# Optimization experiments

Hardware: AMD Instinct MI355X
Metric: run time of the kernel (lower is better)

The kernel has to match this reference:

```python
import jax, jax.numpy as jnp
import numpy as np
import math

B, P, PIX, D, C = 128, 256, 256, 512, 10
MAX_STEPS, TOL, EPS = 4, 1e-3, 1e-5


def setup_inputs() -> dict:
    key = jax.random.key(0)
    ks = jax.random.split(key, 12)
    pi = math.pi
    return {
        "x": jax.random.normal(ks[0], (B, P, PIX), jnp.float32),
        "Wp": jax.random.normal(ks[1], (D, PIX), jnp.float32) * (1.0 / math.sqrt(PIX)),
        "bp": jnp.zeros((D,), jnp.float32),
        "q_rot": jax.random.uniform(ks[2], (D,), jnp.float32, -pi, pi),
        "k_rot": jax.random.uniform(ks[3], (D,), jnp.float32, -pi, pi),
        "v_rot": jax.random.uniform(ks[4], (D,), jnp.float32, -pi, pi),
        "ff_real": jax.random.normal(ks[5], (D, D), jnp.float32) * (1.0 / math.sqrt(D)),
        "ff_imag": jax.random.uniform(ks[6], (D, D), jnp.float32, -0.01, 0.01),
        "Wr": jax.random.normal(ks[7], (C, D), jnp.float32) * 0.05,
        "br": jnp.zeros((C,), jnp.float32),
        "Wi": jax.random.normal(ks[8], (C, D), jnp.float32) * 0.05,
        "bi": jnp.zeros((C,), jnp.float32),
    }


def _complex_norm(x):
    # normalize magnitude stats over last dim, preserve phase (torch.std uses ddof=1)
    mag = jnp.abs(x)
    mean_mag = jnp.mean(mag, axis=-1, keepdims=True)
    std_mag = jnp.std(mag, axis=-1, keepdims=True, ddof=1)
    norm_mag = (mag - mean_mag) / (std_mag + EPS)
    scale = jnp.tanh(norm_mag) / (mag + EPS)
    return x * scale


def _fro(z):
    return jnp.sqrt(jnp.sum(jnp.abs(z) ** 2))


def _pos_phase():
    pos = jnp.arange(P, dtype=jnp.float32)[:, None]
    dim = jnp.arange(D, dtype=jnp.float32)[None, :]
    freq = 1.0 / (10000.0 ** (dim / D))
    return pos * freq * math.pi  # (P, D)


def reference(x, Wp, bp, q_rot, k_rot, v_rot, ff_real, ff_imag, Wr, br, Wi, bi):
    mag = jnp.tanh(jnp.einsum('bpi,di->bpd', x, Wp) + bp)
    state = mag.astype(jnp.complex64) * jnp.exp(1j * _pos_phase())[None]  # (B,P,D)
    ff = (ff_real + 1j * ff_imag).astype(jnp.complex64)
    eq, ek, ev = jnp.exp(1j * q_rot), jnp.exp(1j * k_rot), jnp.exp(1j * v_rot)
    scale = 8.0 / math.sqrt(D)
    active = jnp.array(True)
    for _ in range(MAX_STEPS):  # fixed small iteration count; updates frozen after convergence
        prev = state
        q, k, v = state * eq, state * ek, state * ev
        interference = jnp.einsum('bpd,bqd->bpq', q, jnp.conj(k))
        attn = jax.nn.softmax(interference.real * scale, axis=-1)
        attn_out = jnp.einsum('bpq,bqd->bpd', attn.astype(jnp.complex64), v)
        new_state = _complex_norm((prev + attn_out) @ ff)
        diff = _fro(new_state - prev) / (_fro(new_state) + 1e-8)
        state = jnp.where(active, new_state, prev)
        active = jnp.logical_and(active, diff >= TOL)
    pooled = jnp.mean(state, axis=1)  # (B,D) complex
    logits = pooled.real @ Wr.T + br + pooled.imag @ Wi.T + bi
    return logits
```

## Files before the change

kernel.cpp:

```cpp
#include <hip/hip_runtime.h>
#include <math.h>

#define BB   128
#define PP   256
#define PIX_ 256
#define DD   512
#define CC   10
#define MTOT (BB*PP)
#define NK   1024
#define KA   2048
#define KB2  2048
#define NSLOT (MTOT/4)

static constexpr float SCALE_F = 0.35355339059327373f;
static constexpr float PI_F    = 3.14159265358979323846f;

typedef short bf16x8 __attribute__((ext_vector_type(8)));
typedef float f32x4  __attribute__((ext_vector_type(4)));
typedef unsigned short ushort8 __attribute__((ext_vector_type(8)));

__device__ __forceinline__ unsigned short f2bf(float f) {
    union { float f; unsigned u; } v; v.f = f;
    unsigned r = v.u + 0x7FFF + ((v.u >> 16) & 1);
    return (unsigned short)(r >> 16);
}
__device__ __forceinline__ float bf2f(unsigned short h) {
    union { unsigned u; float f; } v; v.u = ((unsigned)h) << 16;
    return v.f;
}

typedef __attribute__((address_space(3))) unsigned lds_u32;
typedef __attribute__((address_space(1))) const unsigned glb_u32;
__device__ __forceinline__ void gl2lds16(const unsigned short* g, short* l) {
    __builtin_amdgcn_global_load_lds((glb_u32*)g, (lds_u32*)l, 16, 0, 0);
}

__global__ void k_setup(const float* __restrict__ q_rot, const float* __restrict__ k_rot,
                        const float* __restrict__ v_rot,
                        float* __restrict__ freq, float* __restrict__ cd, float* __restrict__ sd,
                        float* __restrict__ cv, float* __restrict__ sv,
                        int* __restrict__ active) {
    int t = threadIdx.x;
    if (t < DD) {
        freq[t] = expf(-(float)t * (9.210340371976184f / 512.0f));
        float dl = q_rot[t] - k_rot[t];
        cd[t] = cosf(dl);       sd[t] = sinf(dl);
        cv[t] = cosf(v_rot[t]); sv[t] = sinf(v_rot[t]);
    }
    if (t == 0) *active = 1;
}

__global__ __launch_bounds__(256) void k_tab(const float* __restrict__ freq,
                                             float* __restrict__ Tc, float* __restrict__ Ts) {
    const int p = blockIdx.x, t = threadIdx.x;
#pragma unroll
    for (int j = 0; j < 2; j++) {
        const int d = t * 2 + j;
        float s, c; sincosf((float)p * freq[d] * PI_F, &s, &c);
        Tc[(size_t)p * DD + d] = c;
        Ts[(size_t)p * DD + d] = s;
    }
}

__global__ __launch_bounds__(256) void k_prep2(const float* __restrict__ Fr, const float* __restrict__ Fi,
                                               unsigned short* __restrict__ Bt2) {
    const int n = blockIdx.x;
    const int t = threadIdx.x;
    unsigned short* row = Bt2 + (size_t)n * KB2;
#pragma unroll
    for (int j4 = 0; j4 < 4; j4++) {
        const int j = j4 * 256 + t;
        float v;
        if (n < 512) v = (j < 512) ? Fr[(size_t)j * DD + n] : -Fi[(size_t)(j - 512) * DD + n];
        else         v = (j < 512) ? Fi[(size_t)j * DD + (n - 512)] : Fr[(size_t)(j - 512) * DD + (n - 512)];
        const unsigned short hi = f2bf(v);
        row[j] = hi;
        row[NK + j] = f2bf(v - bf2f(hi));
    }
}

#define SCAT4(TILE, V4) do { TILE[lk+0][lrow]=(V4).x; TILE[lk+1][lrow]=(V4).y; \
                             TILE[lk+2][lrow]=(V4).z; TILE[lk+3][lrow]=(V4).w; } while(0)

__global__ __launch_bounds__(256) void k_init(const float* __restrict__ x,
        const float* __restrict__ Wp, const float* __restrict__ bp,
        const float* __restrict__ Tc, const float* __restrict__ Ts,
        float* Sr, float* Si,
        unsigned short* X, unsigned short* Y,
        const float* __restrict__ cd, const float* __restrict__ sd,
        const int packed) {
    __shared__ float As[16][68];
    __shared__ float Bs[16][68];
    const int bm = blockIdx.y * 64, bn = blockIdx.x * 64;
    const int t = threadIdx.x, tx = t & 15, ty = t >> 4;
    const int lrow = t >> 2, lk = (t & 3) * 4;
    float acc[4][4] = {};
    for (int k0 = 0; k0 < PIX_; k0 += 16) {
        const float4 a4 = *(const float4*)(x  + (size_t)(bm + lrow) * PIX_ + k0 + lk);
        const float4 b4 = *(const float4*)(Wp + (size_t)(bn + lrow) * PIX_ + k0 + lk);
        __syncthreads();
        SCAT4(As, a4);
        SCAT4(Bs, b4);
        __syncthreads();
#pragma unroll
        for (int kk = 0; kk < 16; ++kk) {
            const float4 av = *(const float4*)&As[kk][ty * 4];
            const float4 bv = *(const float4*)&Bs[kk][tx * 4];
            const float a[4] = {av.x, av.y, av.z, av.w};
            const float b[4] = {bv.x, bv.y, bv.z, bv.w};
#pragma unroll
            for (int i = 0; i < 4; i++)
#pragma unroll
                for (int j = 0; j < 4; j++) acc[i][j] = fmaf(a[i], b[j], acc[i][j]);
        }
    }
    const float4 cd4 = *(const float4*)(cd + bn + tx * 4);
    const float4 sd4 = *(const float4*)(sd + bn + tx * 4);
    const float cdv[4] = {cd4.x, cd4.y, cd4.z, cd4.w};
    const float sdv[4] = {sd4.x, sd4.y, sd4.z, sd4.w};
#pragma unroll
    for (int i = 0; i < 4; i++) {
        const int m = bm + ty * 4 + i;
        const int p = m & 255;
        const float4 c4 = *(const float4*)(Tc + (size_t)p * DD + bn + tx * 4);
        const float4 s4 = *(const float4*)(Ts + (size_t)p * DD + bn + tx * 4);
        const float cphv[4] = {c4.x, c4.y, c4.z, c4.w};
        const float sphv[4] = {s4.x, s4.y, s4.z, s4.w};
        float srv[4], siv[4];
#pragma unroll
        for (int j = 0; j < 4; j++) {
            const int d = bn + tx * 4 + j;
            const float mg = tanhf(acc[i][j] + bp[d]);
            srv[j] = mg * cphv[j]; siv[j] = mg * sphv[j];
        }
        if (packed) {
            ushort4 xhr, xhi, xlr, xli, yhr, yhi, ylr, yli;
            unsigned short* po[8] = {(unsigned short*)&xhr, (unsigned short*)&xhi,
                                     (unsigned short*)&xlr, (unsigned short*)&xli,
                                     (unsigned short*)&yhr, (unsigned short*)&yhi,
                                     (unsigned short*)&ylr, (unsigned short*)&yli};
#pragma unroll
            for (int j = 0; j < 4; j++) {
                const unsigned short hr = f2bf(srv[j]);
                const unsigned short hi_ = f2bf(siv[j]);
                po[0][j] = hr;  po[2][j] = f2bf(srv[j] - bf2f(hr));
                po[1][j] = hi_; po[3][j] = f2bf(siv[j] - bf2f(hi_));
                const float krr = srv[j] * cdv[j] + siv[j] * sdv[j];
                const float kri = siv[j] * cdv[j] - srv[j] * sdv[j];
                const unsigned short y1 = f2bf(krr);
                const unsigned short y2 = f2bf(kri);
                po[4][j] = y1; po[6][j] = f2bf(krr - bf2f(y1));
                po[5][j] = y2; po[7][j] = f2bf(kri - bf2f(y2));
            }
            unsigned short* xr = X + (size_t)m * KA + bn + tx * 4;
            unsigned short* yr = Y + (size_t)m * KA + bn + tx * 4;
            *(ushort4*)(xr)        = xhr; *(ushort4*)(xr + 512)  = xhi;
            *(ushort4*)(xr + 1024) = xlr; *(ushort4*)(xr + 1536) = xli;
            *(ushort4*)(yr)        = yhr; *(ushort4*)(yr + 512)  = yhi;
            *(ushort4*)(yr + 1024) = ylr; *(ushort4*)(yr + 1536) = yli;
        } else {
            float4 vr, vi;
            float* pvr = (float*)&vr; float* pvi = (float*)&vi;
#pragma unroll
            for (int j = 0; j < 4; j++) { pvr[j] = srv[j]; pvi[j] = siv[j]; }
            *(float4*)(Sr + (size_t)m * DD + bn + tx * 4) = vr;
            *(float4*)(Si + (size_t)m * DD + bn + tx * 4) = vi;
        }
    }
}

__global__ __launch_bounds__(256) void k_xy(const float* __restrict__ Sr, const float* __restrict__ Si,
        const float* __restrict__ cd, const float* __restrict__ sd,
        unsigned short* X, unsigned short* Y,
        const int* __restrict__ active) {
    if (*active == 0) return;
    const int r = blockIdx.x, t = threadIdx.x;
    const size_t base = (size_t)r * DD + 2 * t;
    const float2 s_r = *(const float2*)(Sr + base);
    const float2 s_i = *(const float2*)(Si + base);
    const float2 c2  = *(const float2*)(cd + 2 * t);
    const float2 s2  = *(const float2*)(sd + 2 * t);
    unsigned short* xr = X + (size_t)r * KA;
    unsigned short* yr = Y + (size_t)r * KA;
    const float srv[2] = {s_r.x, s_r.y}, siv[2] = {s_i.x, s_i.y};
    const float cv_[2] = {c2.x, c2.y},  sv_[2] = {s2.x, s2.y};
    ushort2 xh_r, xh_i, xl_r, xl_i, yh_r, yh_i, yl_r, yl_i;
    unsigned short* o[8] = {(unsigned short*)&xh_r, (unsigned short*)&xh_i,
                            (unsigned short*)&xl_r, (unsigned short*)&xl_i,
                            (unsigned short*)&yh_r, (unsigned short*)&yh_i,
                            (unsigned short*)&yl_r, (unsigned short*)&yl_i};
#pragma unroll
    for (int e = 0; e < 2; e++) {
        const unsigned short hr = f2bf(srv[e]);
        const unsigned short hi_ = f2bf(siv[e]);
        o[0][e] = hr;  o[2][e] = f2bf(srv[e] - bf2f(hr));
        o[1][e] = hi_; o[3][e] = f2bf(siv[e] - bf2f(hi_));
        const float krr = srv[e] * cv_[e] + siv[e] * sv_[e];
        const float kri = siv[e] * cv_[e] - srv[e] * sv_[e];
        const unsigned short yh1 = f2bf(krr);
        const unsigned short yh2 = f2bf(kri);
        o[4][e] = yh1; o[6][e] = f2bf(krr - bf2f(yh1));
        o[5][e] = yh2; o[7][e] = f2bf(kri - bf2f(yh2));
    }
    *(ushort2*)(xr + 2 * t)        = xh_r;
    *(ushort2*)(xr + 512 + 2 * t)  = xh_i;
    *(ushort2*)(xr + 1024 + 2 * t) = xl_r;
    *(ushort2*)(xr + 1536 + 2 * t) = xl_i;
    *(ushort2*)(yr + 2 * t)        = yh_r;
    *(ushort2*)(yr + 512 + 2 * t)  = yh_i;
    *(ushort2*)(yr + 1024 + 2 * t) = yl_r;
    *(ushort2*)(yr + 1536 + 2 * t) = yl_i;
}

__global__ __launch_bounds__(256) void k_score_sm(const unsigned short* __restrict__ X,
        const unsigned short* __restrict__ Y,
        unsigned short* __restrict__ Asp, const int* __restrict__ active) {
    if (*active == 0) return;
    __shared__ short SM[20480];
    short* XH = SM;
    short* XL = SM + 2048;
    short* YH = SM + 4096;
    short* YL = SM + 12288;
    const int t = threadIdx.x;
    const int w = t >> 6, L = t & 63;
    const int lane15 = L & 15, quad = L >> 4;
    const int nsm = (int)gridDim.x >> 2;
    const int s   = (int)blockIdx.x & (nsm - 1);
    const int rt  = (int)blockIdx.x / nsm;
    const int bm = s * 256 + rt * 64;
    const int yb = s * 256;
    const int gr = t >> 2, ch = (t & 3) * 8;
    short* XHw = XH + w * 512;
    short* XLw = XL + w * 512;
    short* YHw = YH + w * 512;
    short* YLw = YL + w * 512;
    f32x4 acc[16] = {};
    for (int k0 = 0; k0 < 1024; k0 += 32) {
        __syncthreads();
        gl2lds16(X + (size_t)(bm + gr) * KA + k0 + ch,        XHw);
        gl2lds16(X + (size_t)(bm + gr) * KA + 1024 + k0 + ch, XLw);
#pragma unroll
        for (int ss = 0; ss < 4; ss++) {
            gl2lds16(Y + (size_t)(yb + ss * 64 + gr) * KA + k0 + ch,        YHw + ss * 2048);
            gl2lds16(Y + (size_t)(yb + ss * 64 + gr) * KA + 1024 + k0 + ch, YLw + ss * 2048);
        }
        __syncthreads();
        const bf16x8 xh = *(const bf16x8*)(XH + (w * 16 + lane15) * 32 + quad * 8);
        const bf16x8 xl = *(const bf16x8*)(XL + (w * 16 + lane15) * 32 + quad * 8);
#pragma unroll
        for (int tc = 0; tc < 16; tc++) {
            const bf16x8 yh = *(const bf16x8*)(YH + (tc * 16 + lane15) * 32 + quad * 8);
            acc[tc] = __builtin_amdgcn_mfma_f32_16x16x32_bf16(xh, yh, acc[tc], 0, 0, 0);
            acc[tc] = __builtin_amdgcn_mfma_f32_16x16x32_bf16(xl, yh, acc[tc], 0, 0, 0);
            const bf16x8 yl = *(const bf16x8*)(YL + (tc * 16 + lane15) * 32 + quad * 8);
            acc[tc] = __builtin_amdgcn_mfma_f32_16x16x32_bf16(xh, yl, acc[tc], 0, 0, 0);
        }
    }
#pragma unroll
    for (int tc = 0; tc < 16; tc++) acc[tc] *= SCALE_F;
#pragma unroll
    for (int r = 0; r < 4; r++) {
        float mx = acc[0][r];
#pragma unroll
        for (int tc = 1; tc < 16; tc++) mx = fmaxf(mx, acc[tc][r]);
#pragma unroll
        for (int off = 8; off; off >>= 1) mx = fmaxf(mx, __shfl_xor(mx, off, 64));
        float sum = 0.f;
#pragma unroll
        for (int tc = 0; tc < 16; tc++) { acc[tc][r] = __expf(acc[tc][r] - mx); sum += acc[tc][r]; }
#pragma unroll
        for (int off = 8; off; off >>= 1) sum += __shfl_xor(sum, off, 64);
        const float inv = 1.0f / sum;
#pragma unroll
        for (int tc = 0; tc < 16; tc++) acc[tc][r] *= inv;
    }
    __syncthreads();
#pragma unroll
    for (int h = 0; h < 2; h++) {
        if ((w >> 1) == h) {
#pragma unroll
            for (int r = 0; r < 4; r++) {
                const int lr = (w & 1) * 16 + quad * 4 + r;
#pragma unroll
                for (int tc = 0; tc < 16; tc++) {
                    const float p = acc[tc][r];
                    const unsigned short hi = f2bf(p);
                    SM[lr * 520 + tc * 16 + lane15] = (short)hi;
                    SM[lr * 520 + 256 + tc * 16 + lane15] = (short)f2bf(p - bf2f(hi));
                }
            }
        }
        __syncthreads();
        unsigned short* dst = Asp + (size_t)(bm + h * 32) * 512;
#pragma unroll
        for (int k = 0; k < 8; k++) {
            const int c = t + 256 * k;
            const int row = c >> 6, off = (c & 63) * 8;
            *(ushort8*)(dst + (size_t)c * 8) = *(const ushort8*)&SM[row * 520 + off];
        }
        __syncthreads();
    }
}

__global__ __launch_bounds__(256) void k_attnout_mfma(const unsigned short* __restrict__ Asp,
        const unsigned short* __restrict__ X,
        const float* __restrict__ cv, const float* __restrict__ sv,
        unsigned short* __restrict__ A2, const int* __restrict__ active) {
    if (*active == 0) return;
    __shared__ short AhT[128][32];
    __shared__ short AlT[128][32];
    __shared__ short BH[128][40];
    __shared__ short BL[128][40];
    const int t = threadIdx.x;
    const int w = t >> 6, L = t & 63;
    const int lane15 = L & 15, quad = L >> 4;
    const int bm = blockIdx.x * 128;
    const int bn = blockIdx.y * 64;
    const int sample = blockIdx.x >> 1;
    const int gr = t >> 2, ch = (t & 3) * 8;
    short* AhW0 = &AhT[0][0] + w * 512;
    short* AhW1 = AhW0 + 64 * 32;
    short* AlW0 = &AlT[0][0] + w * 512;
    short* AlW1 = AlW0 + 64 * 32;
    const int nn = t & 127, kh = t >> 7;
    const unsigned short* Bsrc = X + (size_t)sample * PP * KA
                               + ((nn < 64) ? (bn + nn) : (512 + bn + nn - 64));
    f32x4 acc[2][8] = {};
    for (int q0 = 0; q0 < PP; q0 += 32) {
        __syncthreads();
        gl2lds16(Asp + (size_t)(bm + gr) * 512      + q0 + ch,       AhW0);
        gl2lds16(Asp + (size_t)(bm + 64 + gr) * 512 + q0 + ch,       AhW1);
        gl2lds16(Asp + (size_t)(bm + gr) * 512      + 256 + q0 + ch, AlW0);
        gl2lds16(Asp + (size_t)(bm + 64 + gr) * 512 + 256 + q0 + ch, AlW1);
#pragma unroll
        for (int kg = 0; kg < 2; kg++) {
            const int qb = kh * 16 + kg * 8;
            bf16x8 hh, ll;
#pragma unroll
            for (int j = 0; j < 8; j++) {
                const size_t o = (size_t)(q0 + qb + j) * KA;
                hh[j] = (short)Bsrc[o];
                ll[j] = (short)Bsrc[o + 1024];
            }
            *(bf16x8*)&BH[nn][qb] = hh;
            *(bf16x8*)&BL[nn][qb] = ll;
        }
        __syncthreads();
        bf16x8 bh[8];
#pragma unroll
        for (int tc = 0; tc < 8; tc++)
            bh[tc] = *(const bf16x8*)&BH[tc * 16 + lane15][quad * 8];
        bf16x8 afh[2];
#pragma unroll
        for (int tr = 0; tr < 2; tr++) {
            afh[tr] = *(const bf16x8*)&AhT[w * 32 + tr * 16 + lane15][quad * 8];
            const bf16x8 afl = *(const bf16x8*)&AlT[w * 32 + tr * 16 + lane15][quad * 8];
#pragma unroll
            for (int tc = 0; tc < 8; tc++)
                acc[tr][tc] = __builtin_amdgcn_mfma_f32_16x16x32_bf16(afh[tr], bh[tc], acc[tr][tc], 0, 0, 0);
#pragma unroll
            for (int tc = 0; tc < 8; tc++)
                acc[tr][tc] = __builtin_amdgcn_mfma_f32_16x16x32_bf16(afl, bh[tc], acc[tr][tc], 0, 0, 0);
        }
#pragma unroll
        for (int tc = 0; tc < 8; tc++) {
            const bf16x8 bl = *(const bf16x8*)&BL[tc * 16 + lane15][quad * 8];
            acc[0][tc] = __builtin_amdgcn_mfma_f32_16x16x32_bf16(afh[0], bl, acc[0][tc], 0, 0, 0);
            acc[1][tc] = __builtin_amdgcn_mfma_f32_16x16x32_bf16(afh[1], bl, acc[1][tc], 0, 0, 0);
        }
    }
#pragma unroll
    for (int tr = 0; tr < 2; tr++) {
#pragma unroll
        for (int tc = 0; tc < 4; tc++) {
            const int d = bn + tc * 16 + lane15;
            const float cvd = cv[d], svd = sv[d];
#pragma unroll
            for (int r = 0; r < 4; r++) {
                const int m = bm + w * 32 + tr * 16 + quad * 4 + r;
                const unsigned short* xrow = X + (size_t)m * KA + d;
                const float pvr = bf2f(xrow[0])   + bf2f(xrow[1024]);
                const float pvi = bf2f(xrow[512]) + bf2f(xrow[1536]);
                const float wr = acc[tr][tc][r];
                const float wi = acc[tr][tc + 4][r];
                const float tr_ = pvr + (wr * cvd - wi * svd);
                const float ti_ = pvi + (wr * svd + wi * cvd);
                const unsigned short rh = f2bf(tr_);
                const unsigned short ih = f2bf(ti_);
                unsigned short* arow = A2 + (size_t)m * KA;
                arow[d]        = rh;
                arow[512 + d]  = ih;
                arow[1024 + d] = f2bf(tr_ - bf2f(rh));
                arow[1536 + d] = f2bf(ti_ - bf2f(ih));
            }
        }
    }
}

__global__ __launch_bounds__(256) void k_ff_mfma2(const unsigned short* __restrict__ A2,
        const unsigned short* __restrict__ Bt2,
        float* __restrict__ U, const int* __restrict__ active) {
    if (*active == 0) return;
    __shared__ short AH[128][32], AL[128][32];
    __shared__ short BH[128][32], BL[128][32];
    const int t = threadIdx.x;
    const int w = t >> 6, L = t & 63;
    const int lane15 = L & 15, quad = L >> 4;
    const int bm = blockIdx.x * 128, bn = blockIdx.y * 128;
    const int gr = t >> 2, ch = (t & 3) * 8;
    short* AHw = &AH[0][0] + w * 512;
    short* ALw = &AL[0][0] + w * 512;
    short* BHw = &BH[0][0] + w * 512;
    short* BLw = &BL[0][0] + w * 512;
    f32x4 acc[2][8] = {};
    for (int k0 = 0; k0 < 1024; k0 += 32) {
        __syncthreads();
        gl2lds16(A2  + (size_t)(bm + gr) * KA       + k0 + ch,        AHw);
        gl2lds16(A2  + (size_t)(bm + 64 + gr) * KA  + k0 + ch,        AHw + 64 * 32);
        gl2lds16(A2  + (size_t)(bm + gr) * KA       + 1024 + k0 + ch, ALw);
        gl2lds16(A2  + (size_t)(bm + 64 + gr) * KA  + 1024 + k0 + ch, ALw + 64 * 32);
        gl2lds16(Bt2 + (size_t)(bn + gr) * KB2      + k0 + ch,        BHw);
        gl2lds16(Bt2 + (size_t)(bn + 64 + gr) * KB2 + k0 + ch,        BHw + 64 * 32);
        gl2lds16(Bt2 + (size_t)(bn + gr) * KB2      + 1024 + k0 + ch, BLw);
        gl2lds16(Bt2 + (size_t)(bn + 64 + gr) * KB2 + 1024 + k0 + ch, BLw + 64 * 32);
        __syncthreads();
        bf16x8 ah[2], al[2];
#pragma unroll
        for (int tr = 0; tr < 2; tr++) {
            ah[tr] = *(const bf16x8*)&AH[w * 32 + tr * 16 + lane15][quad * 8];
            al[tr] = *(const bf16x8*)&AL[w * 32 + tr * 16 + lane15][quad * 8];
        }
#pragma unroll
        for (int tc = 0; tc < 8; tc++) {
            const bf16x8 bh = *(const bf16x8*)&BH[tc * 16 + lane15][quad * 8];
            acc[0][tc] = __builtin_amdgcn_mfma_f32_16x16x32_bf16(ah[0], bh, acc[0][tc], 0, 0, 0);
            acc[1][tc] = __builtin_amdgcn_mfma_f32_16x16x32_bf16(ah[1], bh, acc[1][tc], 0, 0, 0);
            acc[0][tc] = __builtin_amdgcn_mfma_f32_16x16x32_bf16(al[0], bh, acc[0][tc], 0, 0, 0);
            acc[1][tc] = __builtin_amdgcn_mfma_f32_16x16x32_bf16(al[1], bh, acc[1][tc], 0, 0, 0);
            const bf16x8 bl = *(const bf16x8*)&BL[tc * 16 + lane15][quad * 8];
            acc[0][tc] = __builtin_amdgcn_mfma_f32_16x16x32_bf16(ah[0], bl, acc[0][tc], 0, 0, 0);
            acc[1][tc] = __builtin_amdgcn_mfma_f32_16x16x32_bf16(ah[1], bl, acc[1][tc], 0, 0, 0);
        }
    }
#pragma unroll
    for (int tr = 0; tr < 2; tr++)
#pragma unroll
        for (int tc = 0; tc < 8; tc++) {
            const int n = bn + tc * 16 + lane15;
            const int mbase = bm + w * 32 + tr * 16 + quad * 4;
#pragma unroll
            for (int r = 0; r < 4; r++)
                U[(size_t)(mbase + r) * NK + n] = acc[tr][tc][r];
        }
}

__global__ __launch_bounds__(256) void k_norm(const float* U,
        float* Sr, float* Si,
        float* __restrict__ part,
        unsigned short* X, unsigned short* Y,
        const float* __restrict__ cd, const float* __restrict__ sd,
        const int mode, const int* __restrict__ active) {
    if (*active == 0) return;
    __shared__ float red[8];
    const int t = threadIdx.x, rt = t >> 6, L = t & 63;
    const int row = blockIdx.x * 4 + rt;
    const size_t ub = (size_t)row * NK;
    const size_t base = (size_t)row * DD;
    const float4 ur0 = *(const float4*)(U + ub + 4 * L);
    const float4 ur1 = *(const float4*)(U + ub + 256 + 4 * L);
    const float4 ui0 = *(const float4*)(U + ub + 512 + 4 * L);
    const float4 ui1 = *(const float4*)(U + ub + 768 + 4 * L);
    float prr[8], pii[8];
    unsigned short* xr = X + (size_t)row * KA;
    if (mode == 2) {
        const ushort4 hr0 = *(const ushort4*)(xr + 4 * L);
        const ushort4 hr1 = *(const ushort4*)(xr + 256 + 4 * L);
        const ushort4 hi0 = *(const ushort4*)(xr + 512 + 4 * L);
        const ushort4 hi1 = *(const ushort4*)(xr + 768 + 4 * L);
        const ushort4 lr0 = *(const ushort4*)(xr + 1024 + 4 * L);
        const ushort4 lr1 = *(const ushort4*)(xr + 1280 + 4 * L);
        const ushort4 li0 = *(const ushort4*)(xr + 1536 + 4 * L);
        const ushort4 li1 = *(const ushort4*)(xr + 1792 + 4 * L);
        const unsigned short* hr[2] = {(const unsigned short*)&hr0, (const unsigned short*)&hr1};
        const unsigned short* hi[2] = {(const unsigned short*)&hi0, (const unsigned short*)&hi1};
        const unsigned short* lr[2] = {(const unsigned short*)&lr0, (const unsigned short*)&lr1};
        const unsigned short* li[2] = {(const unsigned short*)&li0, (const unsigned short*)&li1};
#pragma unroll
        for (int e = 0; e < 8; e++) {
            const int g = e >> 2, j = e & 3;
            prr[e] = bf2f(hr[g][j]) + bf2f(lr[g][j]);
            pii[e] = bf2f(hi[g][j]) + bf2f(li[g][j]);
        }
    } else {
        const float4 pr0 = *(const float4*)(Sr + base + 4 * L);
        const float4 pr1 = *(const float4*)(Sr + base + 256 + 4 * L);
        const float4 pi0 = *(const float4*)(Si + base + 4 * L);
        const float4 pi1 = *(const float4*)(Si + base + 256 + 4 * L);
        prr[0] = pr0.x; prr[1] = pr0.y; prr[2] = pr0.z; prr[3] = pr0.w;
        prr[4] = pr1.x; prr[5] = pr1.y; prr[6] = pr1.z; prr[7] = pr1.w;
        pii[0] = pi0.x; pii[1] = pi0.y; pii[2] = pi0.z; pii[3] = pi0.w;
        pii[4] = pi1.x; pii[5] = pi1.y; pii[6] = pi1.z; pii[7] = pi1.w;
    }
    const float urr[8] = {ur0.x, ur0.y, ur0.z, ur0.w, ur1.x, ur1.y, ur1.z, ur1.w};
    const float uii[8] = {ui0.x, ui0.y, ui0.z, ui0.w, ui1.x, ui1.y, ui1.z, ui1.w};
    float mg[8], msum = 0.f;
#pragma unroll
    for (int e = 0; e < 8; e++) {
        mg[e] = sqrtf(urr[e] * urr[e] + uii[e] * uii[e]);
        msum += mg[e];
    }
#pragma unroll
    for (int off = 32; off; off >>= 1) msum += __shfl_xor(msum, off, 64);
    const float mean = msum * (1.0f / 512.0f);
    float vs = 0.f;
#pragma unroll
    for (int e = 0; e < 8; e++) { const float d = mg[e] - mean; vs += d * d; }
#pragma unroll
    for (int off = 32; off; off >>= 1) vs += __shfl_xor(vs, off, 64);
    const float istd = 1.0f / (sqrtf(vs * (1.0f / 511.0f)) + 1e-5f);
    float nr[8], ni[8];
#pragma unroll
    for (int e = 0; e < 8; e++) {
        const float sc = tanhf((mg[e] - mean) * istd) / (mg[e] + 1e-5f);
        nr[e] = urr[e] * sc; ni[e] = uii[e] * sc;
    }
    float dd = 0.f, nn = 0.f;
#pragma unroll
    for (int e = 0; e < 8; e++) {
        const float dr = nr[e] - prr[e], di = ni[e] - pii[e];
        dd += dr * dr + di * di;
        nn += nr[e] * nr[e] + ni[e] * ni[e];
    }
    if (mode != 2) {
        *(float4*)(Sr + base + 4 * L)       = make_float4(nr[0], nr[1], nr[2], nr[3]);
        *(float4*)(Sr + base + 256 + 4 * L) = make_float4(nr[4], nr[5], nr[6], nr[7]);
        *(float4*)(Si + base + 4 * L)       = make_float4(ni[0], ni[1], ni[2], ni[3]);
        *(float4*)(Si + base + 256 + 4 * L) = make_float4(ni[4], ni[5], ni[6], ni[7]);
    }
    if (mode >= 1) {
        unsigned short* yr = Y + (size_t)row * KA;
        const float4 c0 = *(const float4*)(cd + 4 * L);
        const float4 c1 = *(const float4*)(cd + 256 + 4 * L);
        const float4 s0 = *(const float4*)(sd + 4 * L);
        const float4 s1 = *(const float4*)(sd + 256 + 4 * L);
        const float cdv[8] = {c0.x, c0.y, c0.z, c0.w, c1.x, c1.y, c1.z, c1.w};
        const float sdv[8] = {s0.x, s0.y, s0.z, s0.w, s1.x, s1.y, s1.z, s1.w};
        ushort4 xhr[2], xhi[2], xlr[2], xli[2], yhr[2], yhi[2], ylr[2], yli[2];
#pragma unroll
        for (int e = 0; e < 8; e++) {
            const int g = e >> 2, j = e & 3;
            const unsigned short hr_ = f2bf(nr[e]);
            const unsigned short hi_ = f2bf(ni[e]);
            ((unsigned short*)&xhr[g])[j] = hr_;
            ((unsigned short*)&xlr[g])[j] = f2bf(nr[e] - bf2f(hr_));
            ((unsigned short*)&xhi[g])[j] = hi_;
            ((unsigned short*)&xli[g])[j] = f2bf(ni[e] - bf2f(hi_));
            const float krr = nr[e] * cdv[e] + ni[e] * sdv[e];
            const float kri = ni[e] * cdv[e] - nr[e] * sdv[e];
            const unsigned short k1 = f2bf(krr);
            const unsigned short k2 = f2bf(kri);
            ((unsigned short*)&yhr[g])[j] = k1;
            ((unsigned short*)&ylr[g])[j] = f2bf(krr - bf2f(k1));
            ((unsigned short*)&yhi[g])[j] = k2;
            ((unsigned short*)&yli[g])[j] = f2bf(kri - bf2f(k2));
        }
        *(ushort4*)(xr + 4 * L)        = xhr[0]; *(ushort4*)(xr + 256 + 4 * L)  = xhr[1];
        *(ushort4*)(xr + 512 + 4 * L)  = xhi[0]; *(ushort4*)(xr + 768 + 4 * L)  = xhi[1];
        *(ushort4*)(xr + 1024 + 4 * L) = xlr[0]; *(ushort4*)(xr + 1280 + 4 * L) = xlr[1];
        *(ushort4*)(xr + 1536 + 4 * L) = xli[0]; *(ushort4*)(xr + 1792 + 4 * L) = xli[1];
        *(ushort4*)(yr + 4 * L)        = yhr[0]; *(ushort4*)(yr + 256 + 4 * L)  = yhr[1];
        *(ushort4*)(yr + 512 + 4 * L)  = yhi[0]; *(ushort4*)(yr + 768 + 4 * L)  = yhi[1];
        *(ushort4*)(yr + 1024 + 4 * L) = ylr[0]; *(ushort4*)(yr + 1280 + 4 * L) = ylr[1];
        *(ushort4*)(yr + 1536 + 4 * L) = yli[0]; *(ushort4*)(yr + 1792 + 4 * L) = yli[1];
    }
#pragma unroll
    for (int off = 32; off; off >>= 1) {
        dd += __shfl_xor(dd, off, 64);
        nn += __shfl_xor(nn, off, 64);
    }
    if (L == 0) { red[rt] = dd; red[4 + rt] = nn; }
    __syncthreads();
    if (t == 0)
        *(float2*)(part + 2 * blockIdx.x) =
            make_float2(red[0] + red[1] + red[2] + red[3],
                        red[4] + red[5] + red[6] + red[7]);
}

__global__ __launch_bounds__(256) void k_flag(const float* __restrict__ part, int* __restrict__ active) {
    __shared__ float red[8];
    const int t = threadIdx.x, rt = t >> 6, L = t & 63;
    float dd = 0.f, nn = 0.f;
    for (int i = t; i < NSLOT; i += 256) {
        const float2 p = *(const float2*)(part + 2 * i);
        dd += p.x; nn += p.y;
    }
#pragma unroll
    for (int off = 32; off; off >>= 1) {
        dd += __shfl_xor(dd, off, 64);
        nn += __shfl_xor(nn, off, 64);
    }
    if (L == 0) { red[rt] = dd; red[4 + rt] = nn; }
    __syncthreads();
    if (t == 0) {
        const float d = red[0] + red[1] + red[2] + red[3];
        const float n = red[4] + red[5] + red[6] + red[7];
        const float diff = sqrtf(d) / (sqrtf(n) + 1e-8f);
        const int a = *active;
        *active = (a && (diff >= 1e-3f)) ? 1 : 0;
    }
}

__global__ __launch_bounds__(256) void k_pool(const float* __restrict__ Sr, const float* __restrict__ Si,
        const unsigned short* __restrict__ X,
        float* __restrict__ Pr, float* __restrict__ Pi, const int packed) {
    const int gid = blockIdx.x * 256 + threadIdx.x;
    const int b = gid >> 9, d = gid & 511;
    float sr = 0.f, si = 0.f;
    if (packed) {
        const unsigned short* xb = X + ((size_t)b * PP) * KA + d;
        for (int p = 0; p < PP; p++) {
            const unsigned short* xr = xb + (size_t)p * KA;
            sr += bf2f(xr[0])   + bf2f(xr[1024]);
            si += bf2f(xr[512]) + bf2f(xr[1536]);
        }
    } else {
        const size_t base = (size_t)b * PP * DD + d;
        for (int p = 0; p < PP; p++) {
            sr += Sr[base + (size_t)p * DD];
            si += Si[base + (size_t)p * DD];
        }
    }
    Pr[gid] = sr * (1.0f / 256.0f);
    Pi[gid] = si * (1.0f / 256.0f);
}

__global__ __launch_bounds__(64) void k_logits(const float* __restrict__ Pr, const float* __restrict__ Pi,
        const float* __restrict__ Wr, const float* __restrict__ br,
        const float* __restrict__ Wi, const float* __restrict__ bi,
        float* __restrict__ out) {
    const int b = blockIdx.x;
    const int lane = threadIdx.x;
    for (int c = 0; c < CC; c++) {
        float acc = 0.f;
#pragma unroll
        for (int k = 0; k < 8; k++) {
            const int d = lane + 64 * k;
            acc += Pr[b * DD + d] * Wr[c * DD + d] + Pi[b * DD + d] * Wi[c * DD + d];
        }
#pragma unroll
        for (int off = 32; off; off >>= 1) acc += __shfl_xor(acc, off, 64);
        if (lane == 0) out[b * CC + c] = acc + br[c] + bi[c];
    }
}

extern "C" void kernel_launch(void* const* d_in, const int* in_sizes, int n_in,
                              void* d_out, int out_size, void* d_ws, size_t ws_size,
                              hipStream_t stream) {
    const float* x     = (const float*)d_in[0];
    const float* Wp    = (const float*)d_in[1];
    const float* bp    = (const float*)d_in[2];
    const float* q_rot = (const float*)d_in[3];
    const float* k_rot = (const float*)d_in[4];
    const float* v_rot = (const float*)d_in[5];
    const float* ffr   = (const float*)d_in[6];
    const float* ffi   = (const float*)d_in[7];
    const float* Wr    = (const float*)d_in[8];
    const float* br    = (const float*)d_in[9];
    const float* Wi    = (const float*)d_in[10];
    const float* bi    = (const float*)d_in[11];
    float* out = (float*)d_out;

    float* ws = (float*)d_ws;
    const size_t plane = (size_t)MTOT * DD;
    const size_t sline = (size_t)PP * DD;

    float* freq = ws;
    float* cd   = freq + DD;
    float* sd   = cd + DD;
    float* cv   = sd + DD;
    float* sv   = cv + DD;
    int*   active = (int*)(sv + DD);
    float* Pr = ws + 4096;
    float* Pi = Pr + (size_t)BB * DD;
    float* part = Pi + (size_t)BB * DD;

    const size_t headf = 151552;
    const size_t btf   = (size_t)NK * KB2 / 2;
    const size_t tabf  = 2 * (size_t)PP * DD;
    const size_t xf    = (size_t)MTOT * KA / 2;
    const size_t packed_f = headf + btf + tabf + 3 * xf;
    const int packed = ((packed_f * 4ull) <= ws_size);

    k_setup<<<1, 512, 0, stream>>>(q_rot, k_rot, v_rot, freq, cd, sd, cv, sv, active);

    if (packed) {
        unsigned short* Bt2 = (unsigned short*)(ws + headf);
        float* Tc = (float*)(Bt2 + (size_t)NK * KB2);
        float* Ts = Tc + (size_t)PP * DD;
        unsigned short* X = (unsigned short*)(Ts + (size_t)PP * DD);
        unsigned short* Y = X + (size_t)MTOT * KA;
        unsigned short* Asp = Y + (size_t)MTOT * KA;
        unsigned short* A2 = Y;
        float* U = (float*)Asp;

        k_tab<<<PP, 256, 0, stream>>>(freq, Tc, Ts);
        k_prep2<<<NK, 256, 0, stream>>>(ffr, ffi, Bt2);
        k_init<<<dim3(DD / 64, MTOT / 64), 256, 0, stream>>>(x, Wp, bp, Tc, Ts,
                nullptr, nullptr, X, Y, cd, sd, 1);

        for (int it = 0; it < 4; ++it) {
            k_score_sm<<<BB * 4, 256, 0, stream>>>(X, Y, Asp, active);
            k_attnout_mfma<<<dim3(BB * 2, 8), 256, 0, stream>>>(Asp, X, cv, sv, A2, active);
            k_ff_mfma2<<<dim3(BB * 2, NK / 128), 256, 0, stream>>>(A2, Bt2, U, active);
            k_norm<<<BB * (PP / 4), 256, 0, stream>>>(U, nullptr, nullptr, part, X, Y, cd, sd, 2, active);
            k_flag<<<1, 256, 0, stream>>>(part, active);
        }
        k_pool<<<BB * DD / 256, 256, 0, stream>>>(nullptr, nullptr, X, Pr, Pi, 1);
    } else {
        float* Sr = part + 2 * NSLOT;
        float* Si = Sr + plane;
        unsigned short* Bt2 = (unsigned short*)(Si + plane);
        float* Tc = (float*)(Bt2 + (size_t)NK * KB2);
        float* Ts = Tc + (size_t)PP * DD;
        float* chunkbase = Si + plane + (size_t)NK * 3072 / 2;

        const size_t fixed_f = (4096 + 2 * (size_t)BB * DD + 2 * NSLOT) + 2 * plane + (size_t)NK * 3072 / 2;
        const size_t perC_f = (size_t)PP * NK * 2 + (size_t)PP * 256;

        int C = BB;
        while (C > 1 && (fixed_f + (size_t)C * perC_f) * 4ull > ws_size) C >>= 1;
        const int fullXY = (C == BB);

        float* U = chunkbase;
        unsigned short* X  = (unsigned short*)chunkbase;
        float* Yf = chunkbase + (size_t)C * PP * NK;
        unsigned short* Y  = (unsigned short*)Yf;
        unsigned short* A2 = Y;
        unsigned short* Asp = (unsigned short*)(Yf + (size_t)C * PP * NK);

        k_tab<<<PP, 256, 0, stream>>>(freq, Tc, Ts);
        k_prep2<<<NK, 256, 0, stream>>>(ffr, ffi, Bt2);
        k_init<<<dim3(DD / 64, MTOT / 64), 256, 0, stream>>>(x, Wp, bp, Tc, Ts,
                Sr, Si, nullptr, nullptr, cd, sd, 0);

        for (int it = 0; it < 4; ++it) {
            for (int c0 = 0; c0 < BB; c0 += C) {
                float* Sr_c = Sr + (size_t)c0 * sline;
                float* Si_c = Si + (size_t)c0 * sline;
                float* part_c = part + (size_t)c0 * (PP / 4) * 2;
                if (!fullXY || it == 0)
                    k_xy<<<C * PP, 256, 0, stream>>>(Sr_c, Si_c, cd, sd, X, Y, active);
                k_score_sm<<<C * 4, 256, 0, stream>>>(X, Y, Asp, active);
                k_attnout_mfma<<<dim3(C * 2, 8), 256, 0, stream>>>(Asp, X, cv, sv, A2, active);
                k_ff_mfma2<<<dim3(C * 2, NK / 128), 256, 0, stream>>>(A2, Bt2, U, active);
                k_norm<<<C * (PP / 4), 256, 0, stream>>>(U, Sr_c, Si_c, part_c, X, Y, cd, sd,
                                                         fullXY ? 1 : 0, active);
            }
            k_flag<<<1, 256, 0, stream>>>(part, active);
        }
        k_pool<<<BB * DD / 256, 256, 0, stream>>>(Sr, Si, nullptr, Pr, Pi, 0);
    }

    k_logits<<<BB, 64, 0, stream>>>(Pr, Pi, Wr, br, Wi, bi, out);
}
```

Baseline: 3.031 ms.

## Rewrite complex FF GEMM as 256x256 double-buffered 8-wave kernel with interleaved staging

Replaces the 128x128 split-bf16 FF GEMM with a 512-thread kernel computing 256x256 tiles over K=64 slices. The three hi/lo product terms become one 3072-long K loop: A runs hi,lo,hi and B runs hi,hi,lo. Global-to-LDS loads for the next slice are double-buffered and interleaved with the MFMA phases, using raised wave priority and partial vmcnt waits. The aim is more data reuse per tile and hiding load latency behind MFMA work. In exchange it needs many more accumulator registers and larger LDS, and the grid shrinks to fewer blocks.

Result: slower. 4.163 ms (+37.4%).

```diff
diff --git a/kernel.cpp b/kernel.cpp
--- a/kernel.cpp
+++ b/kernel.cpp
@@ -33,6 +33,14 @@
 typedef __attribute__((address_space(1))) const unsigned glb_u32;
 __device__ __forceinline__ void gl2lds16(const unsigned short* g, short* l) {
     __builtin_amdgcn_global_load_lds((glb_u32*)g, (lds_u32*)l, 16, 0, 0);
+}
+
+__device__ __forceinline__ void stage_half(const unsigned short* src_base, size_t row_stride,
+                                           int col, short* lds_half, int t) {
+    const int srow = t >> 3, sch = (t & 7) * 8;
+    short* wbase = lds_half + (t >> 6) * 512;
+    gl2lds16(src_base + (size_t)srow * row_stride + col + sch,        wbase);
+    gl2lds16(src_base + (size_t)(64 + srow) * row_stride + col + sch, wbase + 4096);
 }
 
 __global__ void k_setup(const float* __restrict__ q_rot, const float* __restrict__ k_rot,
@@ -397,60 +405,123 @@
     }
 }
 
-__global__ __launch_bounds__(256) void k_ff_mfma2(const unsigned short* __restrict__ A2,
+__global__ __launch_bounds__(512, 2) void k_ff8(const unsigned short* __restrict__ A2,
         const unsigned short* __restrict__ Bt2,
         float* __restrict__ U, const int* __restrict__ active) {
     if (*active == 0) return;
-    __shared__ short AH[128][32], AL[128][32];
-    __shared__ short BH[128][32], BL[128][32];
+    __shared__ short LAs[2][2][128][64];
+    __shared__ short LBs[2][2][128][64];
     const int t = threadIdx.x;
     const int w = t >> 6, L = t & 63;
     const int lane15 = L & 15, quad = L >> 4;
-    const int bm = blockIdx.x * 128, bn = blockIdx.y * 128;
-    const int gr = t >> 2, ch = (t & 3) * 8;
-    short* AHw = &AH[0][0] + w * 512;
-    short* ALw = &AL[0][0] + w * 512;
-    short* BHw = &BH[0][0] + w * 512;
-    short* BLw = &BL[0][0] + w * 512;
-    f32x4 acc[2][8] = {};
-    for (int k0 = 0; k0 < 1024; k0 += 32) {
-        __syncthreads();
-        gl2lds16(A2  + (size_t)(bm + gr) * KA       + k0 + ch,        AHw);
-        gl2lds16(A2  + (size_t)(bm + 64 + gr) * KA  + k0 + ch,        AHw + 64 * 32);
-        gl2lds16(A2  + (size_t)(bm + gr) * KA       + 1024 + k0 + ch, ALw);
-        gl2lds16(A2  + (size_t)(bm + 64 + gr) * KA  + 1024 + k0 + ch, ALw + 64 * 32);
-        gl2lds16(Bt2 + (size_t)(bn + gr) * KB2      + k0 + ch,        BHw);
-        gl2lds16(Bt2 + (size_t)(bn + 64 + gr) * KB2 + k0 + ch,        BHw + 64 * 32);
-        gl2lds16(Bt2 + (size_t)(bn + gr) * KB2      + 1024 + k0 + ch, BLw);
-        gl2lds16(Bt2 + (size_t)(bn + 64 + gr) * KB2 + 1024 + k0 + ch, BLw + 64 * 32);
-        __syncthreads();
-        bf16x8 ah[2], al[2];
-#pragma unroll
-        for (int tr = 0; tr < 2; tr++) {
-            ah[tr] = *(const bf16x8*)&AH[w * 32 + tr * 16 + lane15][quad * 8];
-            al[tr] = *(const bf16x8*)&AL[w * 32 + tr * 16 + lane15][quad * 8];
-        }
-#pragma unroll
-        for (int tc = 0; tc < 8; tc++) {
-            const bf16x8 bh = *(const bf16x8*)&BH[tc * 16 + lane15][quad * 8];
-            acc[0][tc] = __builtin_amdgcn_mfma_f32_16x16x32_bf16(ah[0], bh, acc[0][tc], 0, 0, 0);
-            acc[1][tc] = __builtin_amdgcn_mfma_f32_16x16x32_bf16(ah[1], bh, acc[1][tc], 0, 0, 0);
-            acc[0][tc] = __builtin_amdgcn_mfma_f32_16x16x32_bf16(al[0], bh, acc[0][tc], 0, 0, 0);
-            acc[1][tc] = __builtin_amdgcn_mfma_f32_16x16x32_bf16(al[1], bh, acc[1][tc], 0, 0, 0);
-            const bf16x8 bl = *(const bf16x8*)&BL[tc * 16 + lane15][quad * 8];
-            acc[0][tc] = __builtin_amdgcn_mfma_f32_16x16x32_bf16(ah[0], bl, acc[0][tc], 0, 0, 0);
-            acc[1][tc] = __builtin_amdgcn_mfma_f32_16x16x32_bf16(ah[1], bl, acc[1][tc], 0, 0, 0);
-        }
-    }
-#pragma unroll
-    for (int tr = 0; tr < 2; tr++)
-#pragma unroll
-        for (int tc = 0; tc < 8; tc++) {
-            const int n = bn + tc * 16 + lane15;
-            const int mbase = bm + w * 32 + tr * 16 + quad * 4;
+    const int wr = w >> 2, wc = w & 3;
+    const int bm = blockIdx.x * 256, bn = blockIdx.y * 256;
+
+    f32x4 acc[8][4] = {};
+
+    stage_half(A2  + (size_t)bm * KA,          KA,  0,  &LAs[0][0][0][0], t);
+    stage_half(A2  + (size_t)(bm + 128) * KA,  KA,  0,  &LAs[0][1][0][0], t);
+    stage_half(Bt2 + (size_t)bn * KB2,         KB2, 0,  &LBs[0][0][0][0], t);
+    stage_half(Bt2 + (size_t)(bn + 128) * KB2, KB2, 0,  &LBs[0][1][0][0], t);
+    stage_half(Bt2 + (size_t)bn * KB2,         KB2, 64, &LBs[1][0][0][0], t);
+    stage_half(Bt2 + (size_t)(bn + 128) * KB2, KB2, 64, &LBs[1][1][0][0], t);
+    asm volatile("s_waitcnt vmcnt(0)" ::: "memory");
+    __builtin_amdgcn_s_barrier();
+
+    bf16x8 af[4][2], bf[4][2];
+    const int brow = (wc & 1) * 64;
+    for (int kt = 0; kt < 48; kt++) {
+        const int sl = kt & 1, sn = sl ^ 1;
+        const int ktA = kt + 1, ktB = kt + 2;
+        const int segA = ktA >> 4, kA = (ktA & 15) * 64;
+        const int acolN = (segA == 1) ? 1024 + kA : kA;
+        const int segB = ktB >> 4, kB = (ktB & 15) * 64;
+        const int bcolN = (segB == 2) ? 1024 + kB : kB;
+        const short* LAh = &LAs[sl][wr][0][0];
+        const short* LBh = &LBs[sl][wc >> 1][0][0];
+
+#pragma unroll
+        for (int mf = 0; mf < 4; mf++)
+#pragma unroll
+            for (int ks = 0; ks < 2; ks++)
+                af[mf][ks] = *(const bf16x8*)(LAh + (mf * 16 + lane15) * 64 + ks * 32 + quad * 8);
+#pragma unroll
+        for (int nf = 0; nf < 2; nf++)
+#pragma unroll
+            for (int ks = 0; ks < 2; ks++)
+                bf[nf][ks] = *(const bf16x8*)(LBh + (brow + nf * 16 + lane15) * 64 + ks * 32 + quad * 8);
+        if (ktA < 48) stage_half(A2 + (size_t)bm * KA, KA, acolN, &LAs[sn][0][0][0], t);
+        __builtin_amdgcn_s_barrier();
+        __builtin_amdgcn_s_setprio(1);
+#pragma unroll
+        for (int mf = 0; mf < 4; mf++)
+#pragma unroll
+            for (int nf = 0; nf < 2; nf++)
+#pragma unroll
+                for (int ks = 0; ks < 2; ks++)
+                    acc[mf][nf] = __builtin_amdgcn_mfma_f32_16x16x32_bf16(af[mf][ks], bf[nf][ks], acc[mf][nf], 0, 0, 0);
+        __builtin_amdgcn_s_setprio(0);
+        __builtin_amdgcn_s_barrier();
+
+#pragma unroll
+        for (int nf = 2; nf < 4; nf++)
+#pragma unroll
+            for (int ks = 0; ks < 2; ks++)
+                bf[nf][ks] = *(const bf16x8*)(LBh + (brow + nf * 16 + lane15) * 64 + ks * 32 + quad * 8);
+        if (ktA < 48) stage_half(A2 + (size_t)(bm + 128) * KA, KA, acolN, &LAs[sn][1][0][0], t);
+        __builtin_amdgcn_s_barrier();
+        __builtin_amdgcn_s_setprio(1);
+#pragma unroll
+        for (int mf = 0; mf < 4; mf++)
+#pragma unroll
+            for (int nf = 2; nf < 4; nf++)
+#pragma unroll
+                for (int ks = 0; ks < 2; ks++)
+                    acc[mf][nf] = __builtin_amdgcn_mfma_f32_16x16x32_bf16(af[mf][ks], bf[nf][ks], acc[mf][nf], 0, 0, 0);
+        __builtin_amdgcn_s_setprio(0);
+        __builtin_amdgcn_s_barrier();
+
+#pragma unroll
+        for (int mf = 0; mf < 4; mf++)
+#pragma unroll
+            for (int ks = 0; ks < 2; ks++)
+                af[mf][ks] = *(const bf16x8*)(LAh + ((mf + 4) * 16 + lane15) * 64 + ks * 32 + quad * 8);
+        if (ktB < 48) stage_half(Bt2 + (size_t)bn * KB2, KB2, bcolN, &LBs[sl][0][0][0], t);
+        __builtin_amdgcn_s_barrier();
+        __builtin_amdgcn_s_setprio(1);
+#pragma unroll
+        for (int mf = 0; mf < 4; mf++)
+#pragma unroll
+            for (int nf = 0; nf < 2; nf++)
+#pragma unroll
+                for (int ks = 0; ks < 2; ks++)
+                    acc[mf + 4][nf] = __builtin_amdgcn_mfma_f32_16x16x32_bf16(af[mf][ks], bf[nf][ks], acc[mf + 4][nf], 0, 0, 0);
+        __builtin_amdgcn_s_setprio(0);
+        __builtin_amdgcn_s_barrier();
+
+        if (ktB < 48) stage_half(Bt2 + (size_t)(bn + 128) * KB2, KB2, bcolN, &LBs[sl][1][0][0], t);
+        __builtin_amdgcn_s_barrier();
+        __builtin_amdgcn_s_setprio(1);
+#pragma unroll
+        for (int mf = 0; mf < 4; mf++)
+#pragma unroll
+            for (int nf = 2; nf < 4; nf++)
+#pragma unroll
+                for (int ks = 0; ks < 2; ks++)
+                    acc[mf + 4][nf] = __builtin_amdgcn_mfma_f32_16x16x32_bf16(af[mf][ks], bf[nf][ks], acc[mf + 4][nf], 0, 0, 0);
+        __builtin_amdgcn_s_setprio(0);
+        asm volatile("s_waitcnt vmcnt(4)" ::: "memory");
+        __builtin_amdgcn_s_barrier();
+    }
+#pragma unroll
+    for (int mf = 0; mf < 8; mf++)
+#pragma unroll
+        for (int nf = 0; nf < 4; nf++) {
+            const int n = bn + wc * 64 + nf * 16 + lane15;
+            const int mbase = bm + wr * 128 + mf * 16 + quad * 4;
 #pragma unroll
             for (int r = 0; r < 4; r++)
-                U[(size_t)(mbase + r) * NK + n] = acc[tr][tc][r];
+                U[(size_t)(mbase + r) * NK + n] = acc[mf][nf][r];
         }
 }
 
@@ -711,7 +782,7 @@
         for (int it = 0; it < 4; ++it) {
             k_score_sm<<<BB * 4, 256, 0, stream>>>(X, Y, Asp, active);
             k_attnout_mfma<<<dim3(BB * 2, 8), 256, 0, stream>>>(Asp, X, cv, sv, A2, active);
-            k_ff_mfma2<<<dim3(BB * 2, NK / 128), 256, 0, stream>>>(A2, Bt2, U, active);
+            k_ff8<<<dim3(MTOT / 256, NK / 256), 512, 0, stream>>>(A2, Bt2, U, active);
             k_norm<<<BB * (PP / 4), 256, 0, stream>>>(U, nullptr, nullptr, part, X, Y, cd, sd, 2, active);
             k_flag<<<1, 256, 0, stream>>>(part, active);
         }
@@ -752,7 +823,7 @@
                     k_xy<<<C * PP, 256, 0, stream>>>(Sr_c, Si_c, cd, sd, X, Y, active);
                 k_score_sm<<<C * 4, 256, 0, stream>>>(X, Y, Asp, active);
                 k_attnout_mfma<<<dim3(C * 2, 8), 256, 0, stream>>>(Asp, X, cv, sv, A2, active);
-                k_ff_mfma2<<<dim3(C * 2, NK / 128), 256, 0, stream>>>(A2, Bt2, U, active);
+                k_ff8<<<dim3(C * PP / 256, NK / 256), 512, 0, stream>>>(A2, Bt2, U, active);
                 k_norm<<<C * (PP / 4), 256, 0, stream>>>(U, Sr_c, Si_c, part_c, X, Y, cd, sd,
                                                          fullXY ? 1 : 0, active);
             }
```
